# Kernel optimization log

Measured on AMD Instinct MI355X. Metric: run time of the kernel, lower is better.

## Reference

```python
import jax, jax.numpy as jnp
import numpy as np

FP8_MAX = 448.0


def setup_inputs() -> dict:
    key = jax.random.key(0)
    kx, kw = jax.random.split(key)
    in_features, out_features = 1024, 1024
    x = jax.random.normal(kx, (32768, in_features), dtype=jnp.float32)
    # kaiming_uniform_ with a=sqrt(5): bound = sqrt(6/((1+a^2)*fan_in)) = sqrt(1/fan_in)
    bound = 1.0 / np.sqrt(in_features)
    weight = jax.random.uniform(kw, (out_features, in_features), dtype=jnp.float32,
                                minval=-bound, maxval=bound)
    bias = jnp.zeros((out_features,), dtype=jnp.float32)
    return {"x": x, "weight": weight, "bias": bias}


def reference(x, weight, bias):
    # per-tensor input quant
    input_scale = jnp.maximum(jnp.max(jnp.abs(x)) / FP8_MAX, 1e-12)
    x_q = jnp.round(jnp.clip(x / input_scale, -FP8_MAX, FP8_MAX))
    # per-output-channel weight quant
    weight_amax = jnp.max(jnp.abs(weight), axis=1)            # [out]
    weight_scale = jnp.maximum(weight_amax / FP8_MAX, 1e-12)  # [out]
    weight_q = jnp.round(jnp.clip(weight / weight_scale[:, None], -FP8_MAX, FP8_MAX))
    # integer-valued GEMM in fp32, then dequant + bias
    output_q = jnp.einsum('ti,oi->to', x_q, weight_q)          # [T, out]
    output = output_q * (input_scale * weight_scale)[None, :]
    return output + bias
```

## Files before the change

### kernel.cpp

```cpp
#include <hip/hip_runtime.h>
#include <hip/hip_fp16.h>

#define FP8_MAX 448.0f
#define M_ 32768
#define N_ 1024
#define K_ 1024
#define BM 128
#define BN 128
#define BK 64

typedef _Float16 f16x8 __attribute__((ext_vector_type(8)));
typedef _Float16 f16x4 __attribute__((ext_vector_type(4)));
typedef float f32x4 __attribute__((ext_vector_type(4)));

__device__ inline void gload_lds16(const void* g, void* l) {
    __builtin_amdgcn_global_load_lds(
        (const __attribute__((address_space(1))) void*)g,
        (__attribute__((address_space(3))) void*)l,
        16, 0, 0);
}

__global__ __launch_bounds__(256) void amax_kernel(const float* __restrict__ x,
                                                   unsigned* __restrict__ amax_bits,
                                                   int n) {
    float m = 0.0f;
    const float4* x4 = (const float4*)x;
    int n4 = n >> 2;
    int stride = gridDim.x * blockDim.x;
    for (int i = blockIdx.x * blockDim.x + threadIdx.x; i < n4; i += stride) {
        float4 v = x4[i];
        m = fmaxf(m, fmaxf(fmaxf(fabsf(v.x), fabsf(v.y)),
                           fmaxf(fabsf(v.z), fabsf(v.w))));
    }
    #pragma unroll
    for (int off = 32; off > 0; off >>= 1)
        m = fmaxf(m, __shfl_down(m, off, 64));
    __shared__ float sm[4];
    int lane = threadIdx.x & 63, wv = threadIdx.x >> 6;
    if (lane == 0) sm[wv] = m;
    __syncthreads();
    if (threadIdx.x == 0) {
        float b = fmaxf(fmaxf(sm[0], sm[1]), fmaxf(sm[2], sm[3]));
        atomicMax(amax_bits, __float_as_uint(b));
    }
}

__global__ __launch_bounds__(256) void quant_w_kernel(const float* __restrict__ w,
                                                      float* __restrict__ wscale,
                                                      _Float16* __restrict__ wq) {
    int row = blockIdx.x;
    const float4* wr4 = (const float4*)(w + (size_t)row * K_);
    float4 v = wr4[threadIdx.x];
    float m = fmaxf(fmaxf(fabsf(v.x), fabsf(v.y)), fmaxf(fabsf(v.z), fabsf(v.w)));
    #pragma unroll
    for (int off = 32; off > 0; off >>= 1)
        m = fmaxf(m, __shfl_down(m, off, 64));
    __shared__ float sm[4];
    if ((threadIdx.x & 63) == 0) sm[threadIdx.x >> 6] = m;
    __syncthreads();
    m = fmaxf(fmaxf(sm[0], sm[1]), fmaxf(sm[2], sm[3]));
    float scale = fmaxf(m / FP8_MAX, 1e-12f);
    if (threadIdx.x == 0) wscale[row] = scale;
    float inv = 1.0f / scale;
    f16x4 o;
    o[0] = (_Float16)rintf(fminf(fmaxf(v.x * inv, -FP8_MAX), FP8_MAX));
    o[1] = (_Float16)rintf(fminf(fmaxf(v.y * inv, -FP8_MAX), FP8_MAX));
    o[2] = (_Float16)rintf(fminf(fmaxf(v.z * inv, -FP8_MAX), FP8_MAX));
    o[3] = (_Float16)rintf(fminf(fmaxf(v.w * inv, -FP8_MAX), FP8_MAX));
    ((f16x4*)(wq + (size_t)row * K_))[threadIdx.x] = o;
}

__global__ __launch_bounds__(256) void quant_x_kernel(const float* __restrict__ x,
                                                      const unsigned* __restrict__ amax_bits,
                                                      _Float16* __restrict__ xq,
                                                      int n) {
    float amax = __uint_as_float(*amax_bits);
    float scale = fmaxf(amax / FP8_MAX, 1e-12f);
    float inv = 1.0f / scale;
    const float4* x4 = (const float4*)x;
    f16x4* o4 = (f16x4*)xq;
    int n4 = n >> 2;
    int stride = gridDim.x * blockDim.x;
    for (int i = blockIdx.x * blockDim.x + threadIdx.x; i < n4; i += stride) {
        float4 v = x4[i];
        f16x4 o;
        o[0] = (_Float16)rintf(fminf(fmaxf(v.x * inv, -FP8_MAX), FP8_MAX));
        o[1] = (_Float16)rintf(fminf(fmaxf(v.y * inv, -FP8_MAX), FP8_MAX));
        o[2] = (_Float16)rintf(fminf(fmaxf(v.z * inv, -FP8_MAX), FP8_MAX));
        o[3] = (_Float16)rintf(fminf(fmaxf(v.w * inv, -FP8_MAX), FP8_MAX));
        o4[i] = o;
    }
}

__global__ __launch_bounds__(256) void gemm_kernel(const _Float16* __restrict__ xq,
                                                   const _Float16* __restrict__ wq,
                                                   const unsigned* __restrict__ amax_bits,
                                                   const float* __restrict__ wscale,
                                                   const float* __restrict__ bias,
                                                   float* __restrict__ out) {
    __shared__ __align__(16) _Float16 sA[BM * BK];
    __shared__ __align__(16) _Float16 sB[BN * BK];

    const int tid  = threadIdx.x;
    const int wave = tid >> 6;
    const int lane = tid & 63;
    const int q = lane >> 4;
    const int r = lane & 15;
    const int wm = (wave >> 1) * 64;
    const int wn = (wave & 1) * 64;

    const int m0 = (int)(blockIdx.x >> 3) * BM;
    const int n0 = (int)(blockIdx.x & 7) * BN;

    const int trow = tid >> 3;
    const int tcol = (tid & 7) * 8;

    const _Float16* Ag = xq + ((size_t)(m0 + trow)) * K_ + tcol;
    const _Float16* Bg = wq + ((size_t)(n0 + trow)) * K_ + tcol;
    char* lA = (char*)sA + wave * 1024;
    char* lB = (char*)sB + wave * 1024;

    f32x4 acc[4][4] = {};

    for (int kt = 0; kt < K_; kt += BK) {
        #pragma unroll
        for (int rr = 0; rr < 4; ++rr) {
            gload_lds16(Ag + kt + (size_t)(rr * 32) * K_, lA + rr * 4096);
            gload_lds16(Bg + kt + (size_t)(rr * 32) * K_, lB + rr * 4096);
        }
        __syncthreads();
        #pragma unroll
        for (int kk = 0; kk < BK; kk += 32) {
            f16x8 a[4], b[4];
            #pragma unroll
            for (int i = 0; i < 4; ++i)
                a[i] = *(const f16x8*)&sA[(wm + i * 16 + r) * BK + kk + q * 8];
            #pragma unroll
            for (int j = 0; j < 4; ++j)
                b[j] = *(const f16x8*)&sB[(wn + j * 16 + r) * BK + kk + q * 8];
            #pragma unroll
            for (int i = 0; i < 4; ++i)
                #pragma unroll
                for (int j = 0; j < 4; ++j)
                    acc[i][j] = __builtin_amdgcn_mfma_f32_16x16x32_f16(a[i], b[j], acc[i][j], 0, 0, 0);
        }
        __syncthreads();
    }

    float amax = __uint_as_float(*amax_bits);
    float iscale = fmaxf(amax / FP8_MAX, 1e-12f);

    #pragma unroll
    for (int j = 0; j < 4; ++j) {
        int col = n0 + wn + j * 16 + r;
        float sc = iscale * wscale[col];
        float bs = bias[col];
        #pragma unroll
        for (int i = 0; i < 4; ++i) {
            int rowb = m0 + wm + i * 16 + q * 4;
            #pragma unroll
            for (int t = 0; t < 4; ++t)
                out[(size_t)(rowb + t) * N_ + col] = acc[i][j][t] * sc + bs;
        }
    }
}

extern "C" void kernel_launch(void* const* d_in, const int* in_sizes, int n_in,
                              void* d_out, int out_size, void* d_ws, size_t ws_size,
                              hipStream_t stream) {
    const float* x    = (const float*)d_in[0];
    const float* w    = (const float*)d_in[1];
    const float* bias = (const float*)d_in[2];
    float* out = (float*)d_out;

    char* ws = (char*)d_ws;
    unsigned* amax_bits = (unsigned*)ws;
    float* wscale       = (float*)(ws + 256);
    _Float16* xq        = (_Float16*)(ws + 8192);
    _Float16* wq        = (_Float16*)(ws + 8192 + (size_t)M_ * K_ * 2);

    hipMemsetAsync(amax_bits, 0, 4, stream);
    amax_kernel<<<2048, 256, 0, stream>>>(x, amax_bits, M_ * K_);
    quant_w_kernel<<<1024, 256, 0, stream>>>(w, wscale, wq);
    quant_x_kernel<<<8192, 256, 0, stream>>>(x, amax_bits, xq, M_ * K_);
    gemm_kernel<<<2048, 256, 0, stream>>>(xq, wq, amax_bits, wscale, bias, out);
}
```

Measured before the change: 371.8 us.

## Swizzle GEMM LDS layout, reorder tile mapping, merge amax and weight quant kernels

Applies an XOR swizzle to the 16-byte chunk position in the LDS tiles, on both the global-to-LDS writes and the MFMA operand reads, to reduce LDS bank conflicts. It also changes the block-to-tile mapping so consecutive blocks walk along M with a shared N tile, which changes L2 reuse of the weight tile. The x amax reduction and the weight quantization are merged into one launch to save a kernel launch and let the two run concurrently. The swizzle must match between writer and reader, and the new rasterization may cost some reuse of A.

```diff
diff --git a/kernel.cpp b/kernel.cpp
--- a/kernel.cpp
+++ b/kernel.cpp
@@ -20,54 +20,53 @@
         16, 0, 0);
 }
 
-__global__ __launch_bounds__(256) void amax_kernel(const float* __restrict__ x,
+__global__ __launch_bounds__(256) void prep_kernel(const float* __restrict__ x,
+                                                   const float* __restrict__ w,
                                                    unsigned* __restrict__ amax_bits,
+                                                   float* __restrict__ wscale,
+                                                   _Float16* __restrict__ wq,
                                                    int n) {
-    float m = 0.0f;
-    const float4* x4 = (const float4*)x;
-    int n4 = n >> 2;
-    int stride = gridDim.x * blockDim.x;
-    for (int i = blockIdx.x * blockDim.x + threadIdx.x; i < n4; i += stride) {
-        float4 v = x4[i];
-        m = fmaxf(m, fmaxf(fmaxf(fabsf(v.x), fabsf(v.y)),
-                           fmaxf(fabsf(v.z), fabsf(v.w))));
+    __shared__ float sm[4];
+    if (blockIdx.x < 1024) {
+        int row = blockIdx.x;
+        const float4* wr4 = (const float4*)(w + (size_t)row * K_);
+        float4 v = wr4[threadIdx.x];
+        float m = fmaxf(fmaxf(fabsf(v.x), fabsf(v.y)), fmaxf(fabsf(v.z), fabsf(v.w)));
+        #pragma unroll
+        for (int off = 32; off > 0; off >>= 1)
+            m = fmaxf(m, __shfl_down(m, off, 64));
+        if ((threadIdx.x & 63) == 0) sm[threadIdx.x >> 6] = m;
+        __syncthreads();
+        m = fmaxf(fmaxf(sm[0], sm[1]), fmaxf(sm[2], sm[3]));
+        float scale = fmaxf(m / FP8_MAX, 1e-12f);
+        if (threadIdx.x == 0) wscale[row] = scale;
+        float inv = 1.0f / scale;
+        f16x4 o;
+        o[0] = (_Float16)rintf(fminf(fmaxf(v.x * inv, -FP8_MAX), FP8_MAX));
+        o[1] = (_Float16)rintf(fminf(fmaxf(v.y * inv, -FP8_MAX), FP8_MAX));
+        o[2] = (_Float16)rintf(fminf(fmaxf(v.z * inv, -FP8_MAX), FP8_MAX));
+        o[3] = (_Float16)rintf(fminf(fmaxf(v.w * inv, -FP8_MAX), FP8_MAX));
+        ((f16x4*)(wq + (size_t)row * K_))[threadIdx.x] = o;
+    } else {
+        float m = 0.0f;
+        const float4* x4 = (const float4*)x;
+        int n4 = n >> 2;
+        int stride = 2048 * 256;
+        for (int i = (blockIdx.x - 1024) * 256 + threadIdx.x; i < n4; i += stride) {
+            float4 v = x4[i];
+            m = fmaxf(m, fmaxf(fmaxf(fabsf(v.x), fabsf(v.y)),
+                               fmaxf(fabsf(v.z), fabsf(v.w))));
+        }
+        #pragma unroll
+        for (int off = 32; off > 0; off >>= 1)
+            m = fmaxf(m, __shfl_down(m, off, 64));
+        if ((threadIdx.x & 63) == 0) sm[threadIdx.x >> 6] = m;
+        __syncthreads();
+        if (threadIdx.x == 0) {
+            float b = fmaxf(fmaxf(sm[0], sm[1]), fmaxf(sm[2], sm[3]));
+            atomicMax(amax_bits, __float_as_uint(b));
+        }
     }
-    #pragma unroll
-    for (int off = 32; off > 0; off >>= 1)
-        m = fmaxf(m, __shfl_down(m, off, 64));
-    __shared__ float sm[4];
-    int lane = threadIdx.x & 63, wv = threadIdx.x >> 6;
-    if (lane == 0) sm[wv] = m;
-    __syncthreads();
-    if (threadIdx.x == 0) {
-        float b = fmaxf(fmaxf(sm[0], sm[1]), fmaxf(sm[2], sm[3]));
-        atomicMax(amax_bits, __float_as_uint(b));
-    }
-}
-
-__global__ __launch_bounds__(256) void quant_w_kernel(const float* __restrict__ w,
-                                                      float* __restrict__ wscale,
-                                                      _Float16* __restrict__ wq) {
-    int row = blockIdx.x;
-    const float4* wr4 = (const float4*)(w + (size_t)row * K_);
-    float4 v = wr4[threadIdx.x];
-    float m = fmaxf(fmaxf(fabsf(v.x), fabsf(v.y)), fmaxf(fabsf(v.z), fabsf(v.w)));
-    #pragma unroll
-    for (int off = 32; off > 0; off >>= 1)
-        m = fmaxf(m, __shfl_down(m, off, 64));
-    __shared__ float sm[4];
-    if ((threadIdx.x & 63) == 0) sm[threadIdx.x >> 6] = m;
-    __syncthreads();
-    m = fmaxf(fmaxf(sm[0], sm[1]), fmaxf(sm[2], sm[3]));
-    float scale = fmaxf(m / FP8_MAX, 1e-12f);
-    if (threadIdx.x == 0) wscale[row] = scale;
-    float inv = 1.0f / scale;
-    f16x4 o;
-    o[0] = (_Float16)rintf(fminf(fmaxf(v.x * inv, -FP8_MAX), FP8_MAX));
-    o[1] = (_Float16)rintf(fminf(fmaxf(v.y * inv, -FP8_MAX), FP8_MAX));
-    o[2] = (_Float16)rintf(fminf(fmaxf(v.z * inv, -FP8_MAX), FP8_MAX));
-    o[3] = (_Float16)rintf(fminf(fmaxf(v.w * inv, -FP8_MAX), FP8_MAX));
-    ((f16x4*)(wq + (size_t)row * K_))[threadIdx.x] = o;
 }
 
 __global__ __launch_bounds__(256) void quant_x_kernel(const float* __restrict__ x,
@@ -106,14 +105,15 @@
     const int lane = tid & 63;
     const int q = lane >> 4;
     const int r = lane & 15;
+    const int r7 = r & 7;
     const int wm = (wave >> 1) * 64;
     const int wn = (wave & 1) * 64;
 
-    const int m0 = (int)(blockIdx.x >> 3) * BM;
-    const int n0 = (int)(blockIdx.x & 7) * BN;
+    const int m0 = (int)(blockIdx.x & 255) * BM;
+    const int n0 = (int)(blockIdx.x >> 8) * BN;
 
     const int trow = tid >> 3;
-    const int tcol = (tid & 7) * 8;
+    const int tcol = (((tid & 7) ^ (trow & 7)) * 8);
 
     const _Float16* Ag = xq + ((size_t)(m0 + trow)) * K_ + tcol;
     const _Float16* Bg = wq + ((size_t)(n0 + trow)) * K_ + tcol;
@@ -132,12 +132,14 @@
         #pragma unroll
         for (int kk = 0; kk < BK; kk += 32) {
             f16x8 a[4], b[4];
+            const int chunk = q + (kk >> 3);
+            const int pos = (chunk ^ r7) * 8;
             #pragma unroll
             for (int i = 0; i < 4; ++i)
-                a[i] = *(const f16x8*)&sA[(wm + i * 16 + r) * BK + kk + q * 8];
+                a[i] = *(const f16x8*)&sA[(wm + i * 16 + r) * BK + pos];
             #pragma unroll
             for (int j = 0; j < 4; ++j)
-                b[j] = *(const f16x8*)&sB[(wn + j * 16 + r) * BK + kk + q * 8];
+                b[j] = *(const f16x8*)&sB[(wn + j * 16 + r) * BK + pos];
             #pragma unroll
             for (int i = 0; i < 4; ++i)
                 #pragma unroll
@@ -180,8 +182,7 @@
     _Float16* wq        = (_Float16*)(ws + 8192 + (size_t)M_ * K_ * 2);
 
     hipMemsetAsync(amax_bits, 0, 4, stream);
-    amax_kernel<<<2048, 256, 0, stream>>>(x, amax_bits, M_ * K_);
-    quant_w_kernel<<<1024, 256, 0, stream>>>(w, wscale, wq);
+    prep_kernel<<<3072, 256, 0, stream>>>(x, w, amax_bits, wscale, wq, M_ * K_);
     quant_x_kernel<<<8192, 256, 0, stream>>>(x, amax_bits, xq, M_ * K_);
     gemm_kernel<<<2048, 256, 0, stream>>>(xq, wq, amax_bits, wscale, bias, out);
 }
```

After: 374.0 us. About the same (+0.6%).
